# Optimization experiments

Hardware: AMD Instinct MI355X
Metric: run time of the kernel (lower is better)

Reference implementation:

```python
import math
import jax, jax.numpy as jnp
import numpy as np

B, D, HEADS, IMG = 8, 512, 8, 32
S = IMG * IMG          # 1024
DH = D // HEADS        # 64


def setup_inputs() -> dict:
    key = jax.random.key(0)
    ks = jax.random.split(key, 10)
    def n(k, shape, scale=1.0):
        return jax.random.normal(k, shape, dtype=jnp.float32) * scale
    w_scale = 1.0 / math.sqrt(D)
    return {
        "xs": n(ks[0], (B, D, IMG, IMG)),
        "xt": n(ks[1], (B, S, D)),
        "Wqs": n(ks[2], (D, D), w_scale),
        "Wks": n(ks[3], (D, D), w_scale),
        "Wvs": n(ks[4], (D, D), w_scale),
        "Wqt": n(ks[5], (D, D), w_scale),
        "Wkt": n(ks[6], (D, D), w_scale),
        "Wvt": n(ks[7], (D, D), w_scale),
        "WK": n(ks[8], (DH, S), 1.0 / math.sqrt(DH)),
        "Wo": n(ks[9], (D, D), w_scale),
    }


def _split_heads(x):
    # [B, S, D] -> [B, H, S, d]
    return x.reshape(B, S, HEADS, DH).transpose(0, 2, 1, 3)


def reference(xs, xt, Wqs, Wks, Wvs, Wqt, Wkt, Wvt, WK, Wo):
    # torch .view: raw reshape of [B, D, IMG, IMG] -> [B, S, D]
    xs2 = xs.reshape(B, S, D)
    q = _split_heads(xs2 @ Wqs) + _split_heads(xt @ Wqt)   # [B,H,S,d]
    k = _split_heads(xs2 @ Wks) + _split_heads(xt @ Wkt)
    v = _split_heads(xs2 @ Wvs) + _split_heads(xt @ Wvt)

    # scores = (QK^T + WK(Q)) / sqrt(d), then causal mask
    bias = jnp.einsum('bhqd,ds->bhqs', q, WK)              # query-dependent bias [B,H,S,S]
    scores = (jnp.einsum('bhqd,bhkd->bhqk', q, k) + bias) / math.sqrt(DH)
    causal = jnp.tril(jnp.ones((S, S), dtype=bool))
    scores = jnp.where(causal[None, None], scores, jnp.float32(-1e9))
    attn = jax.nn.softmax(scores, axis=-1)

    h = jnp.einsum('bhqk,bhkd->bhqd', attn, v)             # [B,H,S,d]
    h = h.transpose(0, 2, 1, 3).reshape(B, S, D)
    out = h @ Wo                                           # [B,S,D]
    # torch .view: raw reshape [B,S,D] -> [B, D, IMG, IMG]
    return out.reshape(B, D, IMG, IMG)
```

## Files before the change

kernel.cpp:

```cpp
#include <hip/hip_runtime.h>
#include <stdint.h>


typedef __bf16 bf16x8 __attribute__((ext_vector_type(8)));
typedef float  f32x4  __attribute__((ext_vector_type(4)));
typedef unsigned short u16x8 __attribute__((ext_vector_type(8)));

#define DEVI __device__ __forceinline__

DEVI unsigned short f2b(float f) {
  union { float f; unsigned u; } v; v.f = f;
  unsigned u = v.u;
  return (unsigned short)((u + 0x7FFFu + ((u >> 16) & 1u)) >> 16);
}

__global__ __launch_bounds__(256) void xconvert_kernel(
    const float* __restrict__ xs, const float* __restrict__ xt,
    unsigned short* __restrict__ Xcat)
{
  int gid = blockIdx.x * 256 + threadIdx.x;
  int m = gid >> 7, c0 = (gid & 127) << 3;
  const float* src = (c0 < 512) ? xs + (size_t)m * 512 + c0
                                : xt + (size_t)m * 512 + (c0 - 512);
  float4 a = *(const float4*)src;
  float4 b = *(const float4*)(src + 4);
  u16x8 o;
  o[0] = f2b(a.x); o[1] = f2b(a.y); o[2] = f2b(a.z); o[3] = f2b(a.w);
  o[4] = f2b(b.x); o[5] = f2b(b.y); o[6] = f2b(b.z); o[7] = f2b(b.w);
  *(u16x8*)&Xcat[(size_t)m * 1024 + c0] = o;
}

__global__ __launch_bounds__(256) void wtrans_kernel(
    const float* __restrict__ Wqs, const float* __restrict__ Wks, const float* __restrict__ Wvs,
    const float* __restrict__ Wqt, const float* __restrict__ Wkt, const float* __restrict__ Wvt,
    const float* __restrict__ Wo,  const float* __restrict__ WK,
    unsigned short* __restrict__ WcatT, unsigned short* __restrict__ WoT,
    float* __restrict__ WKT)
{
  __shared__ __align__(16) char lds_raw[64 * 65 * 4];
  const int t = threadIdx.x;
  const int r = t >> 2, cb = (t & 3) << 4;
  const int mat = blockIdx.z;

  if (mat < 6) {
    const float* W = (mat == 0) ? Wqs : (mat == 1) ? Wqt : (mat == 2) ? Wks
                   : (mat == 3) ? Wkt : (mat == 4) ? Wvs : Wvt;
    const int ktile = blockIdx.x, ctile = blockIdx.y;
    unsigned short (*tile)[66] = (unsigned short (*)[66])lds_raw;
    const float* src = W + (size_t)(ktile * 64 + r) * 512 + ctile * 64 + cb;
#pragma unroll
    for (int i = 0; i < 4; i++) {
      float4 v = *(const float4*)(src + i * 4);
      tile[r][cb + i * 4 + 0] = f2b(v.x); tile[r][cb + i * 4 + 1] = f2b(v.y);
      tile[r][cb + i * 4 + 2] = f2b(v.z); tile[r][cb + i * 4 + 3] = f2b(v.w);
    }
    __syncthreads();
    const int n = ctile * 64 + r;
    const int sec = mat >> 1, half = mat & 1;
    u16x8 o0, o1;
#pragma unroll
    for (int i = 0; i < 8; i++) { o0[i] = tile[cb + i][r]; o1[i] = tile[cb + 8 + i][r]; }
    unsigned short* dst = WcatT + (size_t)(sec * 512 + n) * 1024 + half * 512 + ktile * 64 + cb;
    *(u16x8*)dst = o0; *(u16x8*)(dst + 8) = o1;
  } else if (mat == 6) {
    const int ktile = blockIdx.x, ctile = blockIdx.y;
    unsigned short (*tile)[66] = (unsigned short (*)[66])lds_raw;
    const float* src = Wo + (size_t)(ktile * 64 + r) * 512 + ctile * 64 + cb;
#pragma unroll
    for (int i = 0; i < 4; i++) {
      float4 v = *(const float4*)(src + i * 4);
      tile[r][cb + i * 4 + 0] = f2b(v.x); tile[r][cb + i * 4 + 1] = f2b(v.y);
      tile[r][cb + i * 4 + 2] = f2b(v.z); tile[r][cb + i * 4 + 3] = f2b(v.w);
    }
    __syncthreads();
    const int n = ctile * 64 + r;
    u16x8 o0, o1;
#pragma unroll
    for (int i = 0; i < 8; i++) { o0[i] = tile[cb + i][r]; o1[i] = tile[cb + 8 + i][r]; }
    unsigned short* dst = WoT + (size_t)n * 512 + ktile * 64 + cb;
    *(u16x8*)dst = o0; *(u16x8*)(dst + 8) = o1;
  } else {
    const int st = blockIdx.y * 8 + blockIdx.x;
    if (st >= 16) return;
    float (*tf)[65] = (float (*)[65])lds_raw;
    const float* src = WK + (size_t)r * 1024 + st * 64 + cb;
#pragma unroll
    for (int i = 0; i < 4; i++) {
      float4 v = *(const float4*)(src + i * 4);
      tf[r][cb + i * 4 + 0] = v.x; tf[r][cb + i * 4 + 1] = v.y;
      tf[r][cb + i * 4 + 2] = v.z; tf[r][cb + i * 4 + 3] = v.w;
    }
    __syncthreads();
    const int s = st * 64 + r;
    float* dst = WKT + (size_t)s * 64 + cb;
#pragma unroll
    for (int i = 0; i < 4; i++) {
      float4 v;
      v.x = tf[cb + i * 4 + 0][r]; v.y = tf[cb + i * 4 + 1][r];
      v.z = tf[cb + i * 4 + 2][r]; v.w = tf[cb + i * 4 + 3][r];
      *(float4*)(dst + i * 4) = v;
    }
  }
}

template <int EPI>
__global__ __launch_bounds__(256) void gemm_bt(
    const unsigned short* __restrict__ A, const unsigned short* __restrict__ BT, int K,
    float* __restrict__ Out, const float* __restrict__ WKT,
    unsigned short* __restrict__ Qb, unsigned short* __restrict__ Kb,
    unsigned short* __restrict__ Vb)
{
  __shared__ unsigned short As[2][128 * 32];
  __shared__ unsigned short Bs[2][128 * 32];
  const int t = threadIdx.x;
  const int lane = t & 63, wid = t >> 6;
  const int wr = wid >> 1, wc = wid & 1;
  const int mtile = blockIdx.x, ntile = blockIdx.y;
  const int arow = t >> 2, acol = (t & 3) << 3;
  const int li = lane & 15, g = lane >> 4;

  f32x4 acc[4][4];
#pragma unroll
  for (int i = 0; i < 4; i++)
#pragma unroll
    for (int j = 0; j < 4; j++) acc[i][j] = (f32x4){0.f, 0.f, 0.f, 0.f};

  const unsigned short* aBase = A + (size_t)(mtile * 128 + arow) * K + acol;
  const unsigned short* bBase = BT + (size_t)(ntile * 128 + arow) * K + acol;

  auto STAGE = [&](int k0, int bf) {
    __builtin_amdgcn_global_load_lds(
        (const __attribute__((address_space(1))) void*)(aBase + k0),
        (__attribute__((address_space(3))) void*)&As[bf][wid * 512], 16, 0, 0);
    __builtin_amdgcn_global_load_lds(
        (const __attribute__((address_space(1))) void*)(aBase + (size_t)64 * K + k0),
        (__attribute__((address_space(3))) void*)&As[bf][2048 + wid * 512], 16, 0, 0);
    __builtin_amdgcn_global_load_lds(
        (const __attribute__((address_space(1))) void*)(bBase + k0),
        (__attribute__((address_space(3))) void*)&Bs[bf][wid * 512], 16, 0, 0);
    __builtin_amdgcn_global_load_lds(
        (const __attribute__((address_space(1))) void*)(bBase + (size_t)64 * K + k0),
        (__attribute__((address_space(3))) void*)&Bs[bf][2048 + wid * 512], 16, 0, 0);
  };

  STAGE(0, 0);
  __syncthreads();

  int cur = 0;
  for (int k0 = 0; k0 < K; k0 += 32) {
    if (k0 + 32 < K) STAGE(k0 + 32, cur ^ 1);

    bf16x8 af[4], bfr[4];
#pragma unroll
    for (int fi = 0; fi < 4; fi++)
      af[fi] = *(const bf16x8*)&As[cur][(wr * 64 + fi * 16 + li) * 32 + (g << 3)];
#pragma unroll
    for (int fj = 0; fj < 4; fj++)
      bfr[fj] = *(const bf16x8*)&Bs[cur][(wc * 64 + fj * 16 + li) * 32 + (g << 3)];
    __builtin_amdgcn_s_setprio(1);
#pragma unroll
    for (int fi = 0; fi < 4; fi++)
#pragma unroll
      for (int fj = 0; fj < 4; fj++)
        acc[fi][fj] = __builtin_amdgcn_mfma_f32_16x16x32_bf16(af[fi], bfr[fj], acc[fi][fj], 0, 0, 0);
    __builtin_amdgcn_s_setprio(0);
    __syncthreads();
    cur ^= 1;
  }

  const int lm = g << 2;
  if constexpr (EPI == 0) {
    const float QSCALE = 0.18033688011112042f;
    const int sec = ntile >> 2;
#pragma unroll
    for (int fi = 0; fi < 4; fi++) {
      int mg = mtile * 128 + wr * 64 + fi * 16 + lm;
#pragma unroll
      for (int r = 0; r < 4; r++) {
        int m = mg + r;
        int b = m >> 10, s = m & 1023;
        size_t rowo = ((size_t)b * 8) << 16;
        if (sec == 0) {
#pragma unroll
          for (int fj = 0; fj < 4; fj++) {
            int nn = (ntile & 3) * 128 + wc * 64 + fj * 16 + li;
            ((__bf16*)Qb)[rowo + ((size_t)(nn >> 6) << 16) + (size_t)s * 64 + (nn & 63)] =
                (__bf16)(acc[fi][fj][r] * QSCALE);
          }
        } else if (sec == 1) {
#pragma unroll
          for (int fj = 0; fj < 4; fj++) {
            int nn = (ntile & 3) * 128 + wc * 64 + fj * 16 + li;
            int d = nn & 63;
            ((__bf16*)Kb)[rowo + ((size_t)(nn >> 6) << 16) + (size_t)s * 64 + d] =
                (__bf16)(acc[fi][fj][r] + WKT[(size_t)s * 64 + d]);
          }
        } else {
#pragma unroll
          for (int fj = 0; fj < 4; fj++) {
            int nn = (ntile & 3) * 128 + wc * 64 + fj * 16 + li;
            ((__bf16*)Vb)[rowo + ((size_t)(nn >> 6) << 16) + (size_t)s * 64 + (nn & 63)] =
                (__bf16)acc[fi][fj][r];
          }
        }
      }
    }
  } else {
#pragma unroll
    for (int fi = 0; fi < 4; fi++) {
      int mg = mtile * 128 + wr * 64 + fi * 16 + lm;
#pragma unroll
      for (int r = 0; r < 4; r++) {
        size_t m = (size_t)(mg + r);
#pragma unroll
        for (int fj = 0; fj < 4; fj++) {
          int n = ntile * 128 + wc * 64 + fj * 16 + li;
          Out[m * 512 + n] = acc[fi][fj][r];
        }
      }
    }
  }
}

__global__ __launch_bounds__(256) void vtrans_kernel(const unsigned short* __restrict__ Vrm,
                                                     unsigned short* __restrict__ VT)
{
  __shared__ unsigned short tile[64][65];
  const int bh = blockIdx.y, st = blockIdx.x;
  const unsigned short* src = Vrm + (size_t)bh * 65536 + (size_t)st * 64 * 64;
#pragma unroll
  for (int i = 0; i < 16; i++) {
    int idx = i * 256 + threadIdx.x;
    tile[idx >> 6][idx & 63] = src[idx];
  }
  __syncthreads();
  unsigned short* dst = VT + (size_t)bh * 65536 + st * 64;
#pragma unroll
  for (int i = 0; i < 16; i++) {
    int idx = i * 256 + threadIdx.x;
    int dl = idx >> 6, s = idx & 63;
    dst[(size_t)dl * 1024 + s] = tile[s][dl];
  }
}


#define TILE_A(sc, aq0_, aq1_, mrow, lrow, hacc, ps, pbuf, qb, kvb, isLast)                  \
  {                                                                                          \
    __builtin_amdgcn_s_setprio(1);                                                           \
    _Pragma("unroll")                                                                        \
    for (int tt = 0; tt < 4; tt++) {                                                         \
      f32x4 z = (f32x4){0.f, 0.f, 0.f, 0.f};                                                 \
      z = __builtin_amdgcn_mfma_f32_16x16x32_bf16(aq0_, bk[tt][0], z, 0, 0, 0);              \
      z = __builtin_amdgcn_mfma_f32_16x16x32_bf16(aq1_, bk[tt][1], z, 0, 0, 0);              \
      sc[tt] = z;                                                                            \
    }                                                                                        \
    __builtin_amdgcn_s_setprio(0);                                                           \
    float rm[4] = {-3.0e38f, -3.0e38f, -3.0e38f, -3.0e38f};                                  \
    if (isLast) {                                                                            \
      _Pragma("unroll")                                                                      \
      for (int tt = 0; tt < 4; tt++) {                                                       \
        int kpos = kvb + tt * 16 + li;                                                       \
        _Pragma("unroll")                                                                    \
        for (int r = 0; r < 4; r++) {                                                        \
          float sv = sc[tt][r];                                                              \
          sv = (kpos <= qb + (g << 2) + r) ? sv : -3.0e38f;                                  \
          sc[tt][r] = sv;                                                                    \
          rm[r] = fmaxf(rm[r], sv);                                                          \
        }                                                                                    \
      }                                                                                      \
    } else {                                                                                 \
      _Pragma("unroll")                                                                      \
      for (int tt = 0; tt < 4; tt++)                                                         \
        _Pragma("unroll")                                                                    \
        for (int r = 0; r < 4; r++) rm[r] = fmaxf(rm[r], sc[tt][r]);                         \
    }                                                                                        \
    _Pragma("unroll")                                                                        \
    for (int msk = 1; msk < 16; msk <<= 1)                                                   \
      _Pragma("unroll")                                                                      \
      for (int r = 0; r < 4; r++) rm[r] = fmaxf(rm[r], __shfl_xor(rm[r], msk, 64));          \
    int ok_ = 1;                                                                             \
    _Pragma("unroll")                                                                        \
    for (int r = 0; r < 4; r++) ok_ &= (rm[r] <= mrow[r] + 8.0f);                            \
    if (!__all(ok_)) {                                                                       \
      _Pragma("unroll")                                                                      \
      for (int r = 0; r < 4; r++) {                                                          \
        float mn = fmaxf(mrow[r], rm[r]);                                                    \
        float scl = exp2f(mrow[r] - mn);                                                     \
        mrow[r] = mn; lrow[r] *= scl;                                                        \
        _Pragma("unroll")                                                                    \
        for (int fj = 0; fj < 4; fj++) hacc[fj][r] *= scl;                                   \
      }                                                                                      \
    }                                                                                        \
    _Pragma("unroll")                                                                        \
    for (int r = 0; r < 4; r++) ps[r] = 0.f;                                                 \
    _Pragma("unroll")                                                                        \
    for (int tt = 0; tt < 4; tt++)                                                           \
      _Pragma("unroll")                                                                      \
      for (int r = 0; r < 4; r++) {                                                          \
        float p = exp2f(sc[tt][r] - mrow[r]);                                                \
        ps[r] += p;                                                                          \
        pbuf[((g << 2) + r) * 72 + tt * 16 + li] = f2b(p);                                   \
      }                                                                                      \
  }

#define TILE_B(hacc, ps, lrow, pbuf)                                                         \
  {                                                                                          \
    bf16x8 ap0 = *(const bf16x8*)&pbuf[li * 72 + (g << 3)];                                  \
    bf16x8 ap1 = *(const bf16x8*)&pbuf[li * 72 + 32 + (g << 3)];                             \
    __builtin_amdgcn_s_setprio(1);                                                           \
    _Pragma("unroll")                                                                        \
    for (int fj = 0; fj < 4; fj++) {                                                         \
      hacc[fj] = __builtin_amdgcn_mfma_f32_16x16x32_bf16(ap0, bv[fj][0], hacc[fj], 0, 0, 0); \
      hacc[fj] = __builtin_amdgcn_mfma_f32_16x16x32_bf16(ap1, bv[fj][1], hacc[fj], 0, 0, 0); \
    }                                                                                        \
    __builtin_amdgcn_s_setprio(0);                                                           \
    _Pragma("unroll")                                                                        \
    for (int msk = 1; msk < 16; msk <<= 1)                                                   \
      _Pragma("unroll")                                                                      \
      for (int r = 0; r < 4; r++) ps[r] += __shfl_xor(ps[r], msk, 64);                       \
    _Pragma("unroll")                                                                        \
    for (int r = 0; r < 4; r++) lrow[r] += ps[r];                                            \
  }

__global__ __launch_bounds__(256) void attn_kernel(
    const unsigned short* __restrict__ Q, const unsigned short* __restrict__ Kp,
    const unsigned short* __restrict__ VT, unsigned short* __restrict__ Hout)
{
  __shared__ unsigned short Ksm[2][4096];
  __shared__ unsigned short Vsm[2][4096];
  __shared__ unsigned short P_lds[4][2][16 * 72];

  const int tid = threadIdx.x;
  const int lane = tid & 63, w = tid >> 6;
  const int bx = blockIdx.x;
  const int bh = blockIdx.y;
  const int b = bh >> 3, h = bh & 7;
  const int tl = bx * 4 + w;
  const int th = 63 - tl;
  const int qlo = tl * 16, qhi = th * 16;
  const int clo = bx;
  const int cmax = 15 - bx;
  const int g = lane >> 4, li = lane & 15;

  const unsigned short* Kbh = Kp + (size_t)bh * 65536;
  const unsigned short* Vbh = VT + (size_t)bh * 65536;

  auto STAGE = [&](int c, int bf) {
    int j0 = tid, j1 = tid + 256;
    int r0 = j0 >> 3, s0 = (j0 & 7) ^ (r0 & 7);
    int r1 = j1 >> 3, s1 = (j1 & 7) ^ (r1 & 7);
    __builtin_amdgcn_global_load_lds(
        (const __attribute__((address_space(1))) void*)(Kbh + (size_t)(c * 64 + r0) * 64 + s0 * 8),
        (__attribute__((address_space(3))) void*)&Ksm[bf][w * 512], 16, 0, 0);
    __builtin_amdgcn_global_load_lds(
        (const __attribute__((address_space(1))) void*)(Kbh + (size_t)(c * 64 + r1) * 64 + s1 * 8),
        (__attribute__((address_space(3))) void*)&Ksm[bf][2048 + w * 512], 16, 0, 0);
    __builtin_amdgcn_global_load_lds(
        (const __attribute__((address_space(1))) void*)(Vbh + (size_t)r0 * 1024 + c * 64 + s0 * 8),
        (__attribute__((address_space(3))) void*)&Vsm[bf][w * 512], 16, 0, 0);
    __builtin_amdgcn_global_load_lds(
        (const __attribute__((address_space(1))) void*)(Vbh + (size_t)r1 * 1024 + c * 64 + s1 * 8),
        (__attribute__((address_space(3))) void*)&Vsm[bf][2048 + w * 512], 16, 0, 0);
  };

  const unsigned short* QL = Q + ((size_t)bh * 1024 + qlo) * 64;
  const unsigned short* QH = Q + ((size_t)bh * 1024 + qhi) * 64;
  bf16x8 aqL0 = *(const bf16x8*)&QL[li * 64 + (g << 3)];
  bf16x8 aqL1 = *(const bf16x8*)&QL[li * 64 + 32 + (g << 3)];
  bf16x8 aqH0 = *(const bf16x8*)&QH[li * 64 + (g << 3)];
  bf16x8 aqH1 = *(const bf16x8*)&QH[li * 64 + 32 + (g << 3)];

  f32x4 haccL[4], haccH[4];
#pragma unroll
  for (int fj = 0; fj < 4; fj++) {
    haccL[fj] = (f32x4){0.f, 0.f, 0.f, 0.f};
    haccH[fj] = (f32x4){0.f, 0.f, 0.f, 0.f};
  }
  float mrowL[4] = {-3.0e38f, -3.0e38f, -3.0e38f, -3.0e38f};
  float mrowH[4] = {-3.0e38f, -3.0e38f, -3.0e38f, -3.0e38f};
  float lrowL[4] = {0.f, 0.f, 0.f, 0.f};
  float lrowH[4] = {0.f, 0.f, 0.f, 0.f};

  unsigned short* pbL = &P_lds[w][0][0];
  unsigned short* pbH = &P_lds[w][1][0];

  STAGE(0, 0);
  __syncthreads();

  for (int c = 0; c <= cmax; c++) {
    const int cur = c & 1;
    if (c < cmax) STAGE(c + 1, cur ^ 1);

    bf16x8 bk[4][2];
#pragma unroll
    for (int tt = 0; tt < 4; tt++) {
      int s = tt * 16 + li;
#pragma unroll
      for (int x2 = 0; x2 < 2; x2++)
        bk[tt][x2] = *(const bf16x8*)&Ksm[cur][s * 64 + (((g + 4 * x2) ^ (s & 7)) << 3)];
    }

    const int kvb = c * 64;
    const int loAct = (c <= clo);
    float psL[4], psH[4];
    f32x4 scL[4], scH[4];

    if (loAct) TILE_A(scL, aqL0, aqL1, mrowL, lrowL, haccL, psL, pbL, qlo, kvb, (c == clo));
    TILE_A(scH, aqH0, aqH1, mrowH, lrowH, haccH, psH, pbH, qhi, kvb, (c == cmax));

    asm volatile("s_waitcnt lgkmcnt(0)" ::: "memory");
    __builtin_amdgcn_sched_barrier(0);

    bf16x8 bv[4][2];
#pragma unroll
    for (int fj = 0; fj < 4; fj++) {
      int d = fj * 16 + li;
#pragma unroll
      for (int x2 = 0; x2 < 2; x2++)
        bv[fj][x2] = *(const bf16x8*)&Vsm[cur][d * 64 + (((g + 4 * x2) ^ (d & 7)) << 3)];
    }

    if (loAct) TILE_B(haccL, psL, lrowL, pbL);
    TILE_B(haccH, psH, lrowH, pbH);

    __syncthreads();
  }

  float invL[4], invH[4];
#pragma unroll
  for (int r = 0; r < 4; r++) { invL[r] = 1.0f / lrowL[r]; invH[r] = 1.0f / lrowH[r]; }
#pragma unroll
  for (int fj = 0; fj < 4; fj++)
#pragma unroll
    for (int r = 0; r < 4; r++) {
      int qL = qlo + (g << 2) + r;
      int qH = qhi + (g << 2) + r;
      Hout[((size_t)b * 1024 + qL) * 512 + h * 64 + fj * 16 + li] = f2b(haccL[fj][r] * invL[r]);
      Hout[((size_t)b * 1024 + qH) * 512 + h * 64 + fj * 16 + li] = f2b(haccH[fj][r] * invH[r]);
    }
}

extern "C" void kernel_launch(void* const* d_in, const int* in_sizes, int n_in,
                              void* d_out, int out_size, void* d_ws, size_t ws_size,
                              hipStream_t stream)
{
  const float* xs  = (const float*)d_in[0];
  const float* xt  = (const float*)d_in[1];
  const float* Wqs = (const float*)d_in[2];
  const float* Wks = (const float*)d_in[3];
  const float* Wvs = (const float*)d_in[4];
  const float* Wqt = (const float*)d_in[5];
  const float* Wkt = (const float*)d_in[6];
  const float* Wvt = (const float*)d_in[7];
  const float* WK  = (const float*)d_in[8];
  const float* Wo  = (const float*)d_in[9];
  float* out = (float*)d_out;

  char* ws = (char*)d_ws;
  unsigned short* Xcat  = (unsigned short*)(ws);
  unsigned short* Hout  = (unsigned short*)(ws);
  unsigned short* WcatT = (unsigned short*)(ws + 16777216);
  unsigned short* WoT   = (unsigned short*)(ws + 19922944);
  float*          WKT   = (float*)         (ws + 20447232);
  unsigned short* Qb    = (unsigned short*)(ws + 20709376);
  unsigned short* Kb    = (unsigned short*)(ws + 29097984);
  unsigned short* Vrm   = (unsigned short*)(ws + 37486592);
  unsigned short* VT    = (unsigned short*)(ws + 45875200);

  xconvert_kernel<<<4096, 256, 0, stream>>>(xs, xt, Xcat);
  wtrans_kernel<<<dim3(8, 8, 8), 256, 0, stream>>>(Wqs, Wks, Wvs, Wqt, Wkt, Wvt, Wo, WK,
                                                   WcatT, WoT, WKT);
  gemm_bt<0><<<dim3(64, 12), 256, 0, stream>>>(Xcat, WcatT, 1024, nullptr, WKT, Qb, Kb, Vrm);
  vtrans_kernel<<<dim3(16, 64), 256, 0, stream>>>(Vrm, VT);
  attn_kernel<<<dim3(8, 64), 256, 0, stream>>>(Qb, Kb, VT, Hout);
  gemm_bt<1><<<dim3(64, 4), 256, 0, stream>>>(Hout, WoT, 512, out, nullptr, nullptr, nullptr, nullptr);
}
```

Before: 191.2 us.

## Compute transposed scores and pass P to PV MFMA via permlane swaps

The attention kernel now computes S^T (K as the A operand), so each lane holds one query's scores. That makes the row max and sum reductions mostly in-register, needing only two cross-lane shuffles. Probabilities are packed with v_cvt_pk_bf16_f32 and rearranged with permlane32/16 swaps directly into MFMA A-operand layout, which removes the P round-trip through LDS. The paired lo/hi query-tile load balancing is replaced by one tile per wave on a doubled grid, with blocks ordered heaviest-first. That trades the explicit causal balancing for more blocks and hardware scheduling.

```diff
diff --git a/kernel.cpp b/kernel.cpp
--- a/kernel.cpp
+++ b/kernel.cpp
@@ -12,6 +12,18 @@
   union { float f; unsigned u; } v; v.f = f;
   unsigned u = v.u;
   return (unsigned short)((u + 0x7FFFu + ((u >> 16) & 1u)) >> 16);
+}
+
+DEVI unsigned cvt_pk(float lo, float hi) {
+  unsigned r;
+  asm("v_cvt_pk_bf16_f32 %0, %1, %2" : "=v"(r) : "v"(lo), "v"(hi));
+  return r;
+}
+DEVI void pl32(unsigned &a, unsigned &b) {
+  asm("v_permlane32_swap_b32 %0, %1" : "+v"(a), "+v"(b));
+}
+DEVI void pl16(unsigned &a, unsigned &b) {
+  asm("v_permlane16_swap_b32 %0, %1" : "+v"(a), "+v"(b));
 }
 
 __global__ __launch_bounds__(256) void xconvert_kernel(
@@ -243,103 +255,21 @@
   }
 }
 
-
-#define TILE_A(sc, aq0_, aq1_, mrow, lrow, hacc, ps, pbuf, qb, kvb, isLast)                  \
-  {                                                                                          \
-    __builtin_amdgcn_s_setprio(1);                                                           \
-    _Pragma("unroll")                                                                        \
-    for (int tt = 0; tt < 4; tt++) {                                                         \
-      f32x4 z = (f32x4){0.f, 0.f, 0.f, 0.f};                                                 \
-      z = __builtin_amdgcn_mfma_f32_16x16x32_bf16(aq0_, bk[tt][0], z, 0, 0, 0);              \
-      z = __builtin_amdgcn_mfma_f32_16x16x32_bf16(aq1_, bk[tt][1], z, 0, 0, 0);              \
-      sc[tt] = z;                                                                            \
-    }                                                                                        \
-    __builtin_amdgcn_s_setprio(0);                                                           \
-    float rm[4] = {-3.0e38f, -3.0e38f, -3.0e38f, -3.0e38f};                                  \
-    if (isLast) {                                                                            \
-      _Pragma("unroll")                                                                      \
-      for (int tt = 0; tt < 4; tt++) {                                                       \
-        int kpos = kvb + tt * 16 + li;                                                       \
-        _Pragma("unroll")                                                                    \
-        for (int r = 0; r < 4; r++) {                                                        \
-          float sv = sc[tt][r];                                                              \
-          sv = (kpos <= qb + (g << 2) + r) ? sv : -3.0e38f;                                  \
-          sc[tt][r] = sv;                                                                    \
-          rm[r] = fmaxf(rm[r], sv);                                                          \
-        }                                                                                    \
-      }                                                                                      \
-    } else {                                                                                 \
-      _Pragma("unroll")                                                                      \
-      for (int tt = 0; tt < 4; tt++)                                                         \
-        _Pragma("unroll")                                                                    \
-        for (int r = 0; r < 4; r++) rm[r] = fmaxf(rm[r], sc[tt][r]);                         \
-    }                                                                                        \
-    _Pragma("unroll")                                                                        \
-    for (int msk = 1; msk < 16; msk <<= 1)                                                   \
-      _Pragma("unroll")                                                                      \
-      for (int r = 0; r < 4; r++) rm[r] = fmaxf(rm[r], __shfl_xor(rm[r], msk, 64));          \
-    int ok_ = 1;                                                                             \
-    _Pragma("unroll")                                                                        \
-    for (int r = 0; r < 4; r++) ok_ &= (rm[r] <= mrow[r] + 8.0f);                            \
-    if (!__all(ok_)) {                                                                       \
-      _Pragma("unroll")                                                                      \
-      for (int r = 0; r < 4; r++) {                                                          \
-        float mn = fmaxf(mrow[r], rm[r]);                                                    \
-        float scl = exp2f(mrow[r] - mn);                                                     \
-        mrow[r] = mn; lrow[r] *= scl;                                                        \
-        _Pragma("unroll")                                                                    \
-        for (int fj = 0; fj < 4; fj++) hacc[fj][r] *= scl;                                   \
-      }                                                                                      \
-    }                                                                                        \
-    _Pragma("unroll")                                                                        \
-    for (int r = 0; r < 4; r++) ps[r] = 0.f;                                                 \
-    _Pragma("unroll")                                                                        \
-    for (int tt = 0; tt < 4; tt++)                                                           \
-      _Pragma("unroll")                                                                      \
-      for (int r = 0; r < 4; r++) {                                                          \
-        float p = exp2f(sc[tt][r] - mrow[r]);                                                \
-        ps[r] += p;                                                                          \
-        pbuf[((g << 2) + r) * 72 + tt * 16 + li] = f2b(p);                                   \
-      }                                                                                      \
-  }
-
-#define TILE_B(hacc, ps, lrow, pbuf)                                                         \
-  {                                                                                          \
-    bf16x8 ap0 = *(const bf16x8*)&pbuf[li * 72 + (g << 3)];                                  \
-    bf16x8 ap1 = *(const bf16x8*)&pbuf[li * 72 + 32 + (g << 3)];                             \
-    __builtin_amdgcn_s_setprio(1);                                                           \
-    _Pragma("unroll")                                                                        \
-    for (int fj = 0; fj < 4; fj++) {                                                         \
-      hacc[fj] = __builtin_amdgcn_mfma_f32_16x16x32_bf16(ap0, bv[fj][0], hacc[fj], 0, 0, 0); \
-      hacc[fj] = __builtin_amdgcn_mfma_f32_16x16x32_bf16(ap1, bv[fj][1], hacc[fj], 0, 0, 0); \
-    }                                                                                        \
-    __builtin_amdgcn_s_setprio(0);                                                           \
-    _Pragma("unroll")                                                                        \
-    for (int msk = 1; msk < 16; msk <<= 1)                                                   \
-      _Pragma("unroll")                                                                      \
-      for (int r = 0; r < 4; r++) ps[r] += __shfl_xor(ps[r], msk, 64);                       \
-    _Pragma("unroll")                                                                        \
-    for (int r = 0; r < 4; r++) lrow[r] += ps[r];                                            \
-  }
-
 __global__ __launch_bounds__(256) void attn_kernel(
     const unsigned short* __restrict__ Q, const unsigned short* __restrict__ Kp,
     const unsigned short* __restrict__ VT, unsigned short* __restrict__ Hout)
 {
   __shared__ unsigned short Ksm[2][4096];
   __shared__ unsigned short Vsm[2][4096];
-  __shared__ unsigned short P_lds[4][2][16 * 72];
 
   const int tid = threadIdx.x;
   const int lane = tid & 63, w = tid >> 6;
-  const int bx = blockIdx.x;
+  const int bx = 15 - (int)blockIdx.x;
   const int bh = blockIdx.y;
   const int b = bh >> 3, h = bh & 7;
   const int tl = bx * 4 + w;
-  const int th = 63 - tl;
-  const int qlo = tl * 16, qhi = th * 16;
-  const int clo = bx;
-  const int cmax = 15 - bx;
+  const int qbase = tl * 16;
+  const int nchunk = bx + 1;
   const int g = lane >> 4, li = lane & 15;
 
   const unsigned short* Kbh = Kp + (size_t)bh * 65536;
@@ -363,33 +293,21 @@
         (__attribute__((address_space(3))) void*)&Vsm[bf][2048 + w * 512], 16, 0, 0);
   };
 
-  const unsigned short* QL = Q + ((size_t)bh * 1024 + qlo) * 64;
-  const unsigned short* QH = Q + ((size_t)bh * 1024 + qhi) * 64;
-  bf16x8 aqL0 = *(const bf16x8*)&QL[li * 64 + (g << 3)];
-  bf16x8 aqL1 = *(const bf16x8*)&QL[li * 64 + 32 + (g << 3)];
-  bf16x8 aqH0 = *(const bf16x8*)&QH[li * 64 + (g << 3)];
-  bf16x8 aqH1 = *(const bf16x8*)&QH[li * 64 + 32 + (g << 3)];
-
-  f32x4 haccL[4], haccH[4];
-#pragma unroll
-  for (int fj = 0; fj < 4; fj++) {
-    haccL[fj] = (f32x4){0.f, 0.f, 0.f, 0.f};
-    haccH[fj] = (f32x4){0.f, 0.f, 0.f, 0.f};
-  }
-  float mrowL[4] = {-3.0e38f, -3.0e38f, -3.0e38f, -3.0e38f};
-  float mrowH[4] = {-3.0e38f, -3.0e38f, -3.0e38f, -3.0e38f};
-  float lrowL[4] = {0.f, 0.f, 0.f, 0.f};
-  float lrowH[4] = {0.f, 0.f, 0.f, 0.f};
-
-  unsigned short* pbL = &P_lds[w][0][0];
-  unsigned short* pbH = &P_lds[w][1][0];
+  const unsigned short* Qrow = Q + ((size_t)bh * 1024 + qbase) * 64;
+  bf16x8 aq0 = *(const bf16x8*)&Qrow[li * 64 + (g << 3)];
+  bf16x8 aq1 = *(const bf16x8*)&Qrow[li * 64 + 32 + (g << 3)];
+
+  f32x4 hacc[4];
+#pragma unroll
+  for (int fj = 0; fj < 4; fj++) hacc[fj] = (f32x4){0.f, 0.f, 0.f, 0.f};
+  float mrow = -3.0e38f, lrow = 0.f;
 
   STAGE(0, 0);
   __syncthreads();
 
-  for (int c = 0; c <= cmax; c++) {
+  for (int c = 0; c < nchunk; c++) {
     const int cur = c & 1;
-    if (c < cmax) STAGE(c + 1, cur ^ 1);
+    if (c + 1 < nchunk) STAGE(c + 1, cur ^ 1);
 
     bf16x8 bk[4][2];
 #pragma unroll
@@ -400,16 +318,73 @@
         bk[tt][x2] = *(const bf16x8*)&Ksm[cur][s * 64 + (((g + 4 * x2) ^ (s & 7)) << 3)];
     }
 
-    const int kvb = c * 64;
-    const int loAct = (c <= clo);
-    float psL[4], psH[4];
-    f32x4 scL[4], scH[4];
-
-    if (loAct) TILE_A(scL, aqL0, aqL1, mrowL, lrowL, haccL, psL, pbL, qlo, kvb, (c == clo));
-    TILE_A(scH, aqH0, aqH1, mrowH, lrowH, haccH, psH, pbH, qhi, kvb, (c == cmax));
-
-    asm volatile("s_waitcnt lgkmcnt(0)" ::: "memory");
-    __builtin_amdgcn_sched_barrier(0);
+    f32x4 sc[4];
+    __builtin_amdgcn_s_setprio(1);
+#pragma unroll
+    for (int tt = 0; tt < 4; tt++) {
+      f32x4 z = (f32x4){0.f, 0.f, 0.f, 0.f};
+      z = __builtin_amdgcn_mfma_f32_16x16x32_bf16(bk[tt][0], aq0, z, 0, 0, 0);
+      z = __builtin_amdgcn_mfma_f32_16x16x32_bf16(bk[tt][1], aq1, z, 0, 0, 0);
+      sc[tt] = z;
+    }
+    __builtin_amdgcn_s_setprio(0);
+
+    if (c == nchunk - 1) {
+      const int kb = c * 64 + 4 * g;
+      const int qq = qbase + li;
+#pragma unroll
+      for (int tt = 0; tt < 4; tt++)
+#pragma unroll
+        for (int r = 0; r < 4; r++)
+          sc[tt][r] = (kb + tt * 16 + r <= qq) ? sc[tt][r] : -3.0e38f;
+    }
+
+    float rmA = fmaxf(fmaxf(sc[0][0], sc[0][1]), fmaxf(sc[0][2], sc[0][3]));
+    float rmB = fmaxf(fmaxf(sc[1][0], sc[1][1]), fmaxf(sc[1][2], sc[1][3]));
+    float rmC = fmaxf(fmaxf(sc[2][0], sc[2][1]), fmaxf(sc[2][2], sc[2][3]));
+    float rmD = fmaxf(fmaxf(sc[3][0], sc[3][1]), fmaxf(sc[3][2], sc[3][3]));
+    float rm = fmaxf(fmaxf(rmA, rmB), fmaxf(rmC, rmD));
+    rm = fmaxf(rm, __shfl_xor(rm, 16, 64));
+    rm = fmaxf(rm, __shfl_xor(rm, 32, 64));
+
+    if (!__all(rm <= mrow + 8.0f)) {
+      float mn = fmaxf(mrow, rm);
+      float scl = exp2f(mrow - mn);
+      mrow = mn;
+      lrow *= scl;
+      float s0 = __shfl(scl, 20 * g + 0, 64);
+      float s1 = __shfl(scl, 20 * g + 1, 64);
+      float s2 = __shfl(scl, 20 * g + 2, 64);
+      float s3 = __shfl(scl, 20 * g + 3, 64);
+#pragma unroll
+      for (int fj = 0; fj < 4; fj++) {
+        hacc[fj][0] *= s0; hacc[fj][1] *= s1; hacc[fj][2] *= s2; hacc[fj][3] *= s3;
+      }
+    }
+
+#pragma unroll
+    for (int tt = 0; tt < 4; tt++)
+#pragma unroll
+      for (int r = 0; r < 4; r++) sc[tt][r] = exp2f(sc[tt][r] - mrow);
+    float psA = (sc[0][0] + sc[0][1]) + (sc[0][2] + sc[0][3]);
+    float psB = (sc[1][0] + sc[1][1]) + (sc[1][2] + sc[1][3]);
+    float psC = (sc[2][0] + sc[2][1]) + (sc[2][2] + sc[2][3]);
+    float psD = (sc[3][0] + sc[3][1]) + (sc[3][2] + sc[3][3]);
+    float ps = (psA + psB) + (psC + psD);
+
+    unsigned wpk[4][2];
+#pragma unroll
+    for (int tt = 0; tt < 4; tt++) {
+      wpk[tt][0] = cvt_pk(sc[tt][0], sc[tt][1]);
+      wpk[tt][1] = cvt_pk(sc[tt][2], sc[tt][3]);
+    }
+    unsigned A00 = wpk[0][0], A02 = wpk[1][0]; pl32(A00, A02); pl16(A00, A02);
+    unsigned A01 = wpk[0][1], A03 = wpk[1][1]; pl32(A01, A03); pl16(A01, A03);
+    unsigned A10 = wpk[2][0], A12 = wpk[3][0]; pl32(A10, A12); pl16(A10, A12);
+    unsigned A11 = wpk[2][1], A13 = wpk[3][1]; pl32(A11, A13); pl16(A11, A13);
+    union PW { unsigned u[4]; bf16x8 v; } ap0, ap1;
+    ap0.u[0] = A00; ap0.u[1] = A01; ap0.u[2] = A02; ap0.u[3] = A03;
+    ap1.u[0] = A10; ap1.u[1] = A11; ap1.u[2] = A12; ap1.u[3] = A13;
 
     bf16x8 bv[4][2];
 #pragma unroll
@@ -420,24 +395,34 @@
         bv[fj][x2] = *(const bf16x8*)&Vsm[cur][d * 64 + (((g + 4 * x2) ^ (d & 7)) << 3)];
     }
 
-    if (loAct) TILE_B(haccL, psL, lrowL, pbL);
-    TILE_B(haccH, psH, lrowH, pbH);
+    __builtin_amdgcn_s_setprio(1);
+#pragma unroll
+    for (int fj = 0; fj < 4; fj++) {
+      hacc[fj] = __builtin_amdgcn_mfma_f32_16x16x32_bf16(ap0.v, bv[fj][0], hacc[fj], 0, 0, 0);
+      hacc[fj] = __builtin_amdgcn_mfma_f32_16x16x32_bf16(ap1.v, bv[fj][1], hacc[fj], 0, 0, 0);
+    }
+    __builtin_amdgcn_s_setprio(0);
+
+    ps += __shfl_xor(ps, 16, 64);
+    ps += __shfl_xor(ps, 32, 64);
+    lrow += ps;
 
     __syncthreads();
   }
 
-  float invL[4], invH[4];
-#pragma unroll
-  for (int r = 0; r < 4; r++) { invL[r] = 1.0f / lrowL[r]; invH[r] = 1.0f / lrowH[r]; }
-#pragma unroll
-  for (int fj = 0; fj < 4; fj++)
-#pragma unroll
-    for (int r = 0; r < 4; r++) {
-      int qL = qlo + (g << 2) + r;
-      int qH = qhi + (g << 2) + r;
-      Hout[((size_t)b * 1024 + qL) * 512 + h * 64 + fj * 16 + li] = f2b(haccL[fj][r] * invL[r]);
-      Hout[((size_t)b * 1024 + qH) * 512 + h * 64 + fj * 16 + li] = f2b(haccH[fj][r] * invH[r]);
-    }
+  float inv = 1.0f / lrow;
+  float i0 = __shfl(inv, 20 * g + 0, 64);
+  float i1 = __shfl(inv, 20 * g + 1, 64);
+  float i2 = __shfl(inv, 20 * g + 2, 64);
+  float i3 = __shfl(inv, 20 * g + 3, 64);
+#pragma unroll
+  for (int fj = 0; fj < 4; fj++) {
+    size_t base = ((size_t)b * 1024 + qbase + 4 * g) * 512 + h * 64 + fj * 16 + li;
+    Hout[base +   0] = f2b(hacc[fj][0] * i0);
+    Hout[base + 512] = f2b(hacc[fj][1] * i1);
+    Hout[base + 1024] = f2b(hacc[fj][2] * i2);
+    Hout[base + 1536] = f2b(hacc[fj][3] * i3);
+  }
 }
 
 extern "C" void kernel_launch(void* const* d_in, const int* in_sizes, int n_in,
@@ -472,6 +457,6 @@
                                                    WcatT, WoT, WKT);
   gemm_bt<0><<<dim3(64, 12), 256, 0, stream>>>(Xcat, WcatT, 1024, nullptr, WKT, Qb, Kb, Vrm);
   vtrans_kernel<<<dim3(16, 64), 256, 0, stream>>>(Vrm, VT);
-  attn_kernel<<<dim3(8, 64), 256, 0, stream>>>(Qb, Kb, VT, Hout);
+  attn_kernel<<<dim3(16, 64), 256, 0, stream>>>(Qb, Kb, VT, Hout);
   gemm_bt<1><<<dim3(64, 4), 256, 0, stream>>>(Hout, WoT, 512, out, nullptr, nullptr, nullptr, nullptr);
 }
```

Result: no change. 192.1 us (+0.5%).
